# Kernel tuning notes

Hardware: AMD Instinct MI355X
Metric: run time of the kernel (lower is better)

## Reference

```python
import jax, jax.numpy as jnp
import numpy as np

# ---- t2t / fold geometry (FuseFormer defaults) ----
D_MODEL, HD = 512, 1960
K, S, P = 7, 3, 3            # kernel, stride, padding
H, W = 60, 108               # fold output_size
NH = (H + 2 * P - K) // S + 1  # 20
NW = (W + 2 * P - K) // S + 1  # 36
N_VECS = NH * NW             # 720
C = HD // (K * K)            # 40
HP, WP = H + 2 * P, W + 2 * P

# flat positions in the padded image for each (ki,kj,block_i,block_j)
_ki, _kj, _bi, _bj = np.meshgrid(np.arange(K), np.arange(K), np.arange(NH), np.arange(NW), indexing='ij')
POS = jnp.asarray(((_bi * S + _ki) * WP + (_bj * S + _kj)).reshape(-1))  # (K*K*N_VECS,)

# overlap-add count map (fold of all-ones normalizer), cropped to (H, W)
_cnt = np.zeros(HP * WP, dtype=np.float32)
np.add.at(_cnt, np.asarray(POS), 1.0)
NORM = jnp.asarray(_cnt.reshape(HP, WP)[P:P + H, P:P + W])  # (H, W), all > 0


def _fold_norm_unfold(h):
    # h: (B2, HD, N_VECS) -> fold -> divide by count -> unfold -> (B2, HD, N_VECS)
    B2 = h.shape[0]
    v = h.reshape(B2, C, K * K, N_VECS).reshape(B2, C, -1)
    img = jnp.zeros((B2, C, HP * WP), h.dtype).at[:, :, POS].add(v)
    img = img.reshape(B2, C, HP, WP)[:, :, P:P + H, P:P + W] / NORM  # crop + normalize
    imgp = jnp.pad(img, ((0, 0), (0, 0), (P, P), (P, P)))            # re-pad with zeros
    patches = imgp.reshape(B2, C, HP * WP)[:, :, POS]                # gather (unfold)
    return patches.reshape(B2, HD, N_VECS)


def setup_inputs() -> dict:
    key = jax.random.key(0)
    k1, k2, k3, k4, k5 = jax.random.split(key, 5)
    b, n = 4, 5 * N_VECS  # n = 3600
    return {
        'x': jax.random.normal(k1, (b, n, D_MODEL), jnp.float32),
        'W1': jax.random.normal(k2, (D_MODEL, HD), jnp.float32) * (1.0 / np.sqrt(D_MODEL)),
        'b1': jax.random.normal(k3, (HD,), jnp.float32) * 0.01,
        'W2': jax.random.normal(k4, (HD, D_MODEL), jnp.float32) * (1.0 / np.sqrt(HD)),
        'b2': jax.random.normal(k5, (D_MODEL,), jnp.float32) * 0.01,
    }


def reference(x, W1, b1, W2, b2):
    b, n, _ = x.shape
    h = jnp.einsum('bnd,dh->bnh', x, W1) + b1            # (b, n, HD)
    h = h.reshape(-1, N_VECS, HD).transpose(0, 2, 1)     # (B2, HD, N_VECS)
    h = _fold_norm_unfold(h)
    h = h.transpose(0, 2, 1).reshape(b, n, HD)
    out = jnp.einsum('bnh,hd->bnd', jax.nn.relu(h), W2) + b2  # dropout = identity (eval)
    return out
```

## Files before the change

kernel.cpp:

```cpp
#include <hip/hip_runtime.h>

#define D_MODEL 512
#define HD      1960
#define NPAD    2048
#define NVECS   720
#define MROWS   14400
#define MPAD    14464
#define HP      66
#define WP      114
#define IMGPIX  7524

typedef __bf16 bf16x8 __attribute__((ext_vector_type(8)));
typedef float  f32x4  __attribute__((ext_vector_type(4)));

__device__ __forceinline__ unsigned short f2bf(float f) {
    unsigned u = __builtin_bit_cast(unsigned, f);
    u += 0x7FFFu + ((u >> 16) & 1u);
    return (unsigned short)(u >> 16);
}
__device__ __forceinline__ float bf2f(unsigned short s) {
    unsigned u = ((unsigned)s) << 16;
    return __builtin_bit_cast(float, u);
}

__device__ __forceinline__ void gload_lds16(const unsigned short* g, unsigned short* l) {
    __builtin_amdgcn_global_load_lds(
        (const __attribute__((address_space(1))) unsigned int*)g,
        (__attribute__((address_space(3))) unsigned int*)l,
        16, 0, 0);
}

__global__ void cvt_x(const float* __restrict__ x, unsigned short* __restrict__ xb) {
    size_t i = ((size_t)blockIdx.x * 256 + threadIdx.x) * 4;
    const size_t valid = (size_t)MROWS * D_MODEL;
    if (i >= (size_t)MPAD * D_MODEL) return;
    ushort4 o;
    if (i < valid) {
        float4 v = *(const float4*)(x + i);
        o.x = f2bf(v.x); o.y = f2bf(v.y); o.z = f2bf(v.z); o.w = f2bf(v.w);
    } else {
        o.x = o.y = o.z = o.w = 0;
    }
    *(ushort4*)(xb + i) = o;
}

__global__ void transpose_cvt(const float* __restrict__ src, unsigned short* __restrict__ dst,
                              int srcR, int srcC, int dstR, int dstC) {
    __shared__ float tile[32][33];
    int c0 = blockIdx.x * 32;
    int r0 = blockIdx.y * 32;
    int tx = threadIdx.x, ty = threadIdx.y;
    #pragma unroll
    for (int i = 0; i < 32; i += 8) {
        int sr = c0 + ty + i, sc = r0 + tx;
        tile[ty + i][tx] = (sr < srcR && sc < srcC) ? src[(size_t)sr * srcC + sc] : 0.f;
    }
    __syncthreads();
    #pragma unroll
    for (int i = 0; i < 32; i += 8) {
        int dr = r0 + ty + i, dc = c0 + tx;
        if (dr < dstR && dc < dstC)
            dst[(size_t)dr * dstC + dc] = f2bf(tile[tx][ty + i]);
    }
}

template<int MODE>
__global__ void gemm_bt(const unsigned short* __restrict__ A,
                        const unsigned short* __restrict__ BT,
                        const float* __restrict__ bias,
                        void* __restrict__ Cout,
                        int K, int ldc, int validN, int validM) {
    __shared__ unsigned short smem[128 * 128];
    unsigned short* As = smem;
    unsigned short* Bs = smem + 128 * 64;
    const int t    = threadIdx.x;
    const int wid  = t >> 6, lane = t & 63;
    const int wr   = wid >> 1, wc = wid & 1;
    const int lr   = lane & 15, lh = lane >> 4;
    const int m0   = blockIdx.y * 128, n0 = blockIdx.x * 128;

    f32x4 acc[4][4] = {};

    const unsigned short* Aptr = A  + (size_t)(m0 + (t >> 3)) * K + (t & 7) * 8;
    const unsigned short* Bptr = BT + (size_t)(n0 + (t >> 3)) * K + (t & 7) * 8;
    unsigned short* Asl = As + t * 8;
    unsigned short* Bsl = Bs + t * 8;

    for (int kt = 0; kt < K; kt += 64) {
        #pragma unroll
        for (int i = 0; i < 4; ++i) {
            gload_lds16(Aptr + (size_t)(i * 32) * K + kt, Asl + i * 2048);
            gload_lds16(Bptr + (size_t)(i * 32) * K + kt, Bsl + i * 2048);
        }
        __syncthreads();
        #pragma unroll
        for (int ks = 0; ks < 2; ++ks) {
            bf16x8 a[4], b[4];
            #pragma unroll
            for (int f = 0; f < 4; ++f) {
                a[f] = *(const bf16x8*)&As[(wr * 64 + f * 16 + lr) * 64 + ks * 32 + lh * 8];
                b[f] = *(const bf16x8*)&Bs[(wc * 64 + f * 16 + lr) * 64 + ks * 32 + lh * 8];
            }
            #pragma unroll
            for (int fm = 0; fm < 4; ++fm)
                #pragma unroll
                for (int fn = 0; fn < 4; ++fn)
                    acc[fm][fn] = __builtin_amdgcn_mfma_f32_16x16x32_bf16(
                        a[fm], b[fn], acc[fm][fn], 0, 0, 0);
        }
        __syncthreads();
    }

    if (MODE == 0) {
        #pragma unroll
        for (int fm = 0; fm < 4; ++fm) {
            #pragma unroll
            for (int fn = 0; fn < 4; ++fn) {
                int lcol = wc * 64 + fn * 16 + lr;
                float bv = bias[n0 + lcol];
                #pragma unroll
                for (int j = 0; j < 4; ++j) {
                    int lrow = wr * 64 + fm * 16 + lh * 4 + j;
                    smem[lcol * 128 + (lrow ^ ((lcol & 15) << 3))] =
                        f2bf(acc[fm][fn][j] + bv);
                }
            }
        }
        __syncthreads();
        unsigned short* hT = (unsigned short*)Cout;
        int col = t >> 1, half = t & 1;
        int gcol = n0 + col;
        if (gcol < validN) {
            #pragma unroll
            for (int r = 0; r < 16; ++r) {
                int row = half * 64 + r * 4;
                ushort4 v4 = *(const ushort4*)&smem[col * 128 + (row ^ ((col & 15) << 3))];
                *(ushort4*)&hT[(size_t)gcol * MPAD + m0 + row] = v4;
            }
        }
    } else {
        #pragma unroll
        for (int fm = 0; fm < 4; ++fm) {
            #pragma unroll
            for (int fn = 0; fn < 4; ++fn) {
                int gcol = n0 + wc * 64 + fn * 16 + lr;
                float bv = bias[gcol];
                #pragma unroll
                for (int j = 0; j < 4; ++j) {
                    int grow = m0 + wr * 64 + fm * 16 + lh * 4 + j;
                    if (grow < validM)
                        ((float*)Cout)[(size_t)grow * ldc + gcol] = acc[fm][fn][j] + bv;
                }
            }
        }
    }
}

__global__ void fold_norm(const unsigned short* __restrict__ hT, unsigned short* __restrict__ img2) {
    int y  = blockIdx.x;
    int g  = blockIdx.y;
    int b2 = g / 10, cg = g % 10;
    int c0 = cg * 4;
    int x  = threadIdx.x;
    if (x >= WP) return;
    float val[4] = {0.f, 0.f, 0.f, 0.f};
    if (y >= 3 && y < 63 && x >= 3 && x < 111) {
        int kiA[3], biA[3], nki = 0;
        for (int ki = y % 3; ki < 7; ki += 3) {
            int bi = (y - ki) / 3;
            if (y - ki >= 0 && bi < 20) { kiA[nki] = ki; biA[nki] = bi; ++nki; }
        }
        int kjA[3], bjA[3], nkj = 0;
        for (int kj = x % 3; kj < 7; kj += 3) {
            int bj = (x - kj) / 3;
            if (x - kj >= 0 && bj < 36) { kjA[nkj] = kj; bjA[nkj] = bj; ++nkj; }
        }
        float s[4] = {0.f, 0.f, 0.f, 0.f};
        for (int i = 0; i < nki; ++i) {
            for (int j = 0; j < nkj; ++j) {
                int row = b2 * NVECS + biA[i] * 36 + bjA[j];
                int colb = kiA[i] * 7 + kjA[j];
                #pragma unroll
                for (int q = 0; q < 4; ++q)
                    s[q] += bf2f(hT[(size_t)((c0 + q) * 49 + colb) * MPAD + row]);
            }
        }
        float inv = 1.f / (float)(nki * nkj);
        #pragma unroll
        for (int q = 0; q < 4; ++q)
            val[q] = fmaxf(s[q] * inv, 0.f);
    }
    #pragma unroll
    for (int q = 0; q < 4; ++q)
        img2[(size_t)(b2 * 40 + c0 + q) * IMGPIX + y * WP + x] = f2bf(val[q]);
}

__global__ void unfold_k(const unsigned short* __restrict__ img2, unsigned short* __restrict__ h2b) {
    __shared__ unsigned short lds[20 * 798];
    __shared__ unsigned short lut[980];
    const int gb = blockIdx.x;
    const int cg = blockIdx.y;
    const int b2 = gb / 20, bi = gb % 20;
    const int t  = threadIdx.x;

    const unsigned short* src = img2 + (size_t)(b2 * 40 + cg * 20) * IMGPIX + (bi * 3) * WP;
    for (int p = t; p < 7980; p += 256) {
        int cc = p / 399, rem2 = p - cc * 399;
        *(ushort2*)&lds[cc * 798 + rem2 * 2] =
            *(const ushort2*)&src[(size_t)cc * IMGPIX + rem2 * 2];
    }
    for (int L = t; L < 980; L += 256) {
        int cc = L / 49, kk = L - cc * 49;
        lut[L] = (unsigned short)(cc * 798 + (kk / 7) * 114 + (kk % 7));
    }
    __syncthreads();

    const int cpr   = (cg == 0) ? 245 : 267;
    const int total = 36 * cpr;
    const int rowbase = b2 * NVECS + bi * 36;
    const int hdbase  = cg * 980;
    for (int i = t; i < total; i += 256) {
        int r = i / cpr, q = i - r * cpr;
        int hl = q * 4;
        ushort4 v;
        unsigned short* vv = (unsigned short*)&v;
        #pragma unroll
        for (int e = 0; e < 4; ++e) {
            int h = hl + e;
            vv[e] = (h < 980) ? lds[lut[h] + r * 3] : (unsigned short)0;
        }
        *(ushort4*)&h2b[(size_t)(rowbase + r) * NPAD + hdbase + hl] = v;
    }
}

extern "C" void kernel_launch(void* const* d_in, const int* in_sizes, int n_in,
                              void* d_out, int out_size, void* d_ws, size_t ws_size,
                              hipStream_t stream) {
    const float* x  = (const float*)d_in[0];
    const float* W1 = (const float*)d_in[1];
    const float* b1 = (const float*)d_in[2];
    const float* W2 = (const float*)d_in[3];
    const float* b2 = (const float*)d_in[4];
    float* out = (float*)d_out;

    unsigned short* xb   = (unsigned short*)d_ws;
    unsigned short* W1T  = xb   + (size_t)MPAD * D_MODEL;
    unsigned short* W2T  = W1T  + (size_t)NPAD * D_MODEL;
    unsigned short* hT   = W2T  + (size_t)D_MODEL * NPAD;
    unsigned short* h2b  = hT   + (size_t)NPAD * MPAD;
    unsigned short* img2 = h2b  + (size_t)MPAD * NPAD;

    cvt_x<<<(MPAD * D_MODEL / 4 + 255) / 256, 256, 0, stream>>>(x, xb);

    dim3 tb(32, 8);
    transpose_cvt<<<dim3(512 / 32, NPAD / 32), tb, 0, stream>>>(W1, W1T, D_MODEL, HD, NPAD, D_MODEL);
    transpose_cvt<<<dim3(NPAD / 32, 512 / 32), tb, 0, stream>>>(W2, W2T, HD, D_MODEL, D_MODEL, NPAD);

    gemm_bt<0><<<dim3(NPAD / 128, MPAD / 128), 256, 0, stream>>>(
        xb, W1T, b1, hT, D_MODEL, 0, HD, MPAD);

    fold_norm<<<dim3(HP, 200), 128, 0, stream>>>(hT, img2);
    unfold_k<<<dim3(400, 2), 256, 0, stream>>>(img2, h2b);

    gemm_bt<1><<<dim3(512 / 128, MPAD / 128), 256, 0, stream>>>(
        h2b, W2T, b2, out, NPAD, D_MODEL, D_MODEL, MROWS);
}
```

Before: 188.6 us.

## Use 256x256 double-buffered GEMM tiles and split-K for second GEMM

Both GEMMs move from 128x128 tiles with 256 threads to 256x256 tiles with 512 threads. The kernel double-buffers LDS with XOR-swizzled async global-to-LDS loads and uses explicit vmcnt waits and priority hints so loads overlap MFMA work. The second GEMM is split along K into two halves, with partial fp32 results written into the reused hT workspace and a new combine kernel that adds them together with the bias. MPAD grows so rows are a multiple of 256. In exchange, the 128 KB of LDS per block limits occupancy, and split-K adds extra partial-sum memory traffic plus one more launch.

```diff
diff --git a/kernel.cpp b/kernel.cpp
--- a/kernel.cpp
+++ b/kernel.cpp
@@ -5,7 +5,7 @@
 #define NPAD    2048
 #define NVECS   720
 #define MROWS   14400
-#define MPAD    14464
+#define MPAD    14592
 #define HP      66
 #define WP      114
 #define IMGPIX  7524
@@ -65,94 +65,140 @@
 }
 
 template<int MODE>
-__global__ void gemm_bt(const unsigned short* __restrict__ A,
-                        const unsigned short* __restrict__ BT,
-                        const float* __restrict__ bias,
-                        void* __restrict__ Cout,
-                        int K, int ldc, int validN, int validM) {
-    __shared__ unsigned short smem[128 * 128];
-    unsigned short* As = smem;
-    unsigned short* Bs = smem + 128 * 64;
+__global__ __launch_bounds__(512, 2) void gemm256(const unsigned short* __restrict__ A,
+                         const unsigned short* __restrict__ BT,
+                         const float* __restrict__ bias,
+                         void* __restrict__ Cout,
+                         int K, int NT, int validN) {
+    __shared__ unsigned short lds[65536];
     const int t    = threadIdx.x;
-    const int wid  = t >> 6, lane = t & 63;
-    const int wr   = wid >> 1, wc = wid & 1;
+    const int lane = t & 63;
+    const int wid  = t >> 6;
+    const int wr   = wid >> 2, wc = wid & 3;
     const int lr   = lane & 15, lh = lane >> 4;
-    const int m0   = blockIdx.y * 128, n0 = blockIdx.x * 128;
-
-    f32x4 acc[4][4] = {};
-
-    const unsigned short* Aptr = A  + (size_t)(m0 + (t >> 3)) * K + (t & 7) * 8;
-    const unsigned short* Bptr = BT + (size_t)(n0 + (t >> 3)) * K + (t & 7) * 8;
-    unsigned short* Asl = As + t * 8;
-    unsigned short* Bsl = Bs + t * 8;
-
-    for (int kt = 0; kt < K; kt += 64) {
-        #pragma unroll
-        for (int i = 0; i < 4; ++i) {
-            gload_lds16(Aptr + (size_t)(i * 32) * K + kt, Asl + i * 2048);
-            gload_lds16(Bptr + (size_t)(i * 32) * K + kt, Bsl + i * 2048);
-        }
+    const int m0   = blockIdx.y * 256, n0 = blockIdx.x * 256;
+    const int kz   = (MODE == 1) ? blockIdx.z : 0;
+    const unsigned short* Ab = A  + (size_t)kz * 1024;
+    const unsigned short* Bb = BT + (size_t)kz * 1024;
+
+    const int c0i = t,        r0i = c0i >> 3, q0 = (c0i & 7) ^ (r0i & 7);
+    const int c1i = t + 512,  r1i = c1i >> 3, q1 = (c1i & 7) ^ (r1i & 7);
+    const unsigned soffA00 = (unsigned)((m0 +       r0i) * K + q0 * 8);
+    const unsigned soffA01 = (unsigned)((m0 +       r1i) * K + q1 * 8);
+    const unsigned soffA10 = (unsigned)((m0 + 128 + r0i) * K + q0 * 8);
+    const unsigned soffA11 = (unsigned)((m0 + 128 + r1i) * K + q1 * 8);
+    const unsigned soffB00 = (unsigned)((n0 +       r0i) * K + q0 * 8);
+    const unsigned soffB01 = (unsigned)((n0 +       r1i) * K + q1 * 8);
+    const unsigned soffB10 = (unsigned)((n0 + 128 + r0i) * K + q0 * 8);
+    const unsigned soffB11 = (unsigned)((n0 + 128 + r1i) * K + q1 * 8);
+
+#define STAGE8(buf, kk) do { \
+        unsigned short* L = lds + (buf) * 32768; \
+        gload_lds16(Ab + soffA00 + (kk), L +         t * 8); \
+        gload_lds16(Ab + soffA01 + (kk), L +  4096 + t * 8); \
+        gload_lds16(Ab + soffA10 + (kk), L +  8192 + t * 8); \
+        gload_lds16(Ab + soffA11 + (kk), L + 12288 + t * 8); \
+        gload_lds16(Bb + soffB00 + (kk), L + 16384 +         t * 8); \
+        gload_lds16(Bb + soffB01 + (kk), L + 16384 +  4096 + t * 8); \
+        gload_lds16(Bb + soffB10 + (kk), L + 16384 +  8192 + t * 8); \
+        gload_lds16(Bb + soffB11 + (kk), L + 16384 + 12288 + t * 8); \
+    } while (0)
+
+    f32x4 acc[8][4] = {};
+
+    STAGE8(0, 0);
+    if (NT > 1) STAGE8(1, 64);
+
+    const int sl0 = lh ^ (lr & 7);
+    const int sl1 = sl0 ^ 4;
+
+    for (int kt = 0; kt < NT; ++kt) {
+        const int buf = kt & 1;
+        if (kt + 1 < NT) { asm volatile("s_waitcnt vmcnt(8)" ::: "memory"); }
+        else             { asm volatile("s_waitcnt vmcnt(0)" ::: "memory"); }
+        __builtin_amdgcn_s_barrier();
+        const unsigned short* La = lds + buf * 32768 + wr * 8192;
+        const unsigned short* Lb = lds + buf * 32768 + 16384 + (wc >> 1) * 8192 + (wc & 1) * 4096;
+        #pragma unroll
+        for (int ks = 0; ks < 2; ++ks) {
+            const int sl = ks ? sl1 : sl0;
+            bf16x8 a[8], b[4];
+            #pragma unroll
+            for (int f = 0; f < 8; ++f)
+                a[f] = *(const bf16x8*)(La + (f * 16 + lr) * 64 + sl * 8);
+            #pragma unroll
+            for (int g = 0; g < 4; ++g)
+                b[g] = *(const bf16x8*)(Lb + (g * 16 + lr) * 64 + sl * 8);
+            __builtin_amdgcn_s_setprio(1);
+            #pragma unroll
+            for (int f = 0; f < 8; ++f)
+                #pragma unroll
+                for (int g = 0; g < 4; ++g)
+                    acc[f][g] = __builtin_amdgcn_mfma_f32_16x16x32_bf16(a[f], b[g], acc[f][g], 0, 0, 0);
+            __builtin_amdgcn_s_setprio(0);
+        }
+        __builtin_amdgcn_s_barrier();
+        if (kt + 2 < NT) STAGE8(buf, (kt + 2) * 64);
+    }
+#undef STAGE8
+
+    if (MODE == 0) {
         __syncthreads();
         #pragma unroll
-        for (int ks = 0; ks < 2; ++ks) {
-            bf16x8 a[4], b[4];
-            #pragma unroll
-            for (int f = 0; f < 4; ++f) {
-                a[f] = *(const bf16x8*)&As[(wr * 64 + f * 16 + lr) * 64 + ks * 32 + lh * 8];
-                b[f] = *(const bf16x8*)&Bs[(wc * 64 + f * 16 + lr) * 64 + ks * 32 + lh * 8];
+        for (int f = 0; f < 8; ++f) {
+            #pragma unroll
+            for (int g = 0; g < 4; ++g) {
+                int col = wc * 64 + g * 16 + lr;
+                float bv = bias[n0 + col];
+                int gr = wr * 32 + f * 4 + lh;
+                ushort4 v4;
+                v4.x = f2bf(acc[f][g][0] + bv);
+                v4.y = f2bf(acc[f][g][1] + bv);
+                v4.z = f2bf(acc[f][g][2] + bv);
+                v4.w = f2bf(acc[f][g][3] + bv);
+                *(ushort4*)(lds + col * 256 + ((gr ^ (col & 63)) << 2)) = v4;
             }
-            #pragma unroll
-            for (int fm = 0; fm < 4; ++fm)
-                #pragma unroll
-                for (int fn = 0; fn < 4; ++fn)
-                    acc[fm][fn] = __builtin_amdgcn_mfma_f32_16x16x32_bf16(
-                        a[fm], b[fn], acc[fm][fn], 0, 0, 0);
         }
         __syncthreads();
-    }
-
-    if (MODE == 0) {
-        #pragma unroll
-        for (int fm = 0; fm < 4; ++fm) {
-            #pragma unroll
-            for (int fn = 0; fn < 4; ++fn) {
-                int lcol = wc * 64 + fn * 16 + lr;
-                float bv = bias[n0 + lcol];
+        unsigned short* hT = (unsigned short*)Cout;
+        int col = t & 255, half = t >> 8;
+        int gcol = n0 + col;
+        if (gcol < validN) {
+            #pragma unroll
+            for (int i = 0; i < 32; ++i) {
+                int gr = half * 32 + i;
+                ushort4 v4 = *(const ushort4*)(lds + col * 256 + ((gr ^ (col & 63)) << 2));
+                *(ushort4*)&hT[(size_t)gcol * MPAD + m0 + gr * 4] = v4;
+            }
+        }
+    } else {
+        float* P = (float*)Cout + (size_t)kz * ((size_t)MPAD * 512);
+        #pragma unroll
+        for (int f = 0; f < 8; ++f) {
+            #pragma unroll
+            for (int g = 0; g < 4; ++g) {
+                int gcol = n0 + wc * 64 + g * 16 + lr;
                 #pragma unroll
                 for (int j = 0; j < 4; ++j) {
-                    int lrow = wr * 64 + fm * 16 + lh * 4 + j;
-                    smem[lcol * 128 + (lrow ^ ((lcol & 15) << 3))] =
-                        f2bf(acc[fm][fn][j] + bv);
+                    int grow = m0 + wr * 128 + f * 16 + lh * 4 + j;
+                    P[(size_t)grow * 512 + gcol] = acc[f][g][j];
                 }
             }
         }
-        __syncthreads();
-        unsigned short* hT = (unsigned short*)Cout;
-        int col = t >> 1, half = t & 1;
-        int gcol = n0 + col;
-        if (gcol < validN) {
-            #pragma unroll
-            for (int r = 0; r < 16; ++r) {
-                int row = half * 64 + r * 4;
-                ushort4 v4 = *(const ushort4*)&smem[col * 128 + (row ^ ((col & 15) << 3))];
-                *(ushort4*)&hT[(size_t)gcol * MPAD + m0 + row] = v4;
-            }
-        }
-    } else {
-        #pragma unroll
-        for (int fm = 0; fm < 4; ++fm) {
-            #pragma unroll
-            for (int fn = 0; fn < 4; ++fn) {
-                int gcol = n0 + wc * 64 + fn * 16 + lr;
-                float bv = bias[gcol];
-                #pragma unroll
-                for (int j = 0; j < 4; ++j) {
-                    int grow = m0 + wr * 64 + fm * 16 + lh * 4 + j;
-                    if (grow < validM)
-                        ((float*)Cout)[(size_t)grow * ldc + gcol] = acc[fm][fn][j] + bv;
-                }
-            }
-        }
+    }
+}
+
+__global__ void combine_k(const float* __restrict__ P, const float* __restrict__ bias,
+                          float* __restrict__ out) {
+    const float* P1 = P + (size_t)MPAD * 512;
+    const size_t total = (size_t)MROWS * 512;
+    for (size_t i = ((size_t)blockIdx.x * 256 + threadIdx.x) * 4; i < total;
+         i += (size_t)gridDim.x * 256 * 4) {
+        float4 a = *(const float4*)(P + i);
+        float4 b = *(const float4*)(P1 + i);
+        float4 bv = *(const float4*)(bias + (i & 511));
+        float4 o = {a.x + b.x + bv.x, a.y + b.y + bv.y, a.z + b.z + bv.z, a.w + b.w + bv.w};
+        *(float4*)(out + i) = o;
     }
 }
 
@@ -256,12 +302,13 @@
     transpose_cvt<<<dim3(512 / 32, NPAD / 32), tb, 0, stream>>>(W1, W1T, D_MODEL, HD, NPAD, D_MODEL);
     transpose_cvt<<<dim3(NPAD / 32, 512 / 32), tb, 0, stream>>>(W2, W2T, HD, D_MODEL, D_MODEL, NPAD);
 
-    gemm_bt<0><<<dim3(NPAD / 128, MPAD / 128), 256, 0, stream>>>(
-        xb, W1T, b1, hT, D_MODEL, 0, HD, MPAD);
+    gemm256<0><<<dim3(NPAD / 256, MPAD / 256), 512, 0, stream>>>(
+        xb, W1T, b1, hT, D_MODEL, D_MODEL / 64, HD);
 
     fold_norm<<<dim3(HP, 200), 128, 0, stream>>>(hT, img2);
     unfold_k<<<dim3(400, 2), 256, 0, stream>>>(img2, h2b);
 
-    gemm_bt<1><<<dim3(512 / 128, MPAD / 128), 256, 0, stream>>>(
-        h2b, W2T, b2, out, NPAD, D_MODEL, D_MODEL, MROWS);
-}
+    gemm256<1><<<dim3(D_MODEL / 256, MPAD / 256, 2), 512, 0, stream>>>(
+        h2b, W2T, b2, hT, NPAD, 1024 / 64, D_MODEL);
+    combine_k<<<2048, 256, 0, stream>>>((const float*)hT, b2, out);
+}
```

New measurement: 189.7 us. About the same (+0.6%).

## Double-buffer GEMM LDS tiles with XOR swizzle and prefetch next K-tile

Applied to the files above, without the earlier changes.

The GEMM main loop now uses two LDS buffers. The next K-tile is issued via global-to-LDS loads before the current tile is computed, so memory latency overlaps with MFMA work. The LDS layout is XOR-swizzled on 16-byte chunks to reduce bank conflicts on fragment reads, and MFMA sections raise wave priority with s_setprio. LDS use doubles to 64KB per block, which may reduce occupancy, and the hand-written vmcnt waits assume exactly 8 outstanding loads per stage.

```diff
diff --git a/kernel.cpp b/kernel.cpp
--- a/kernel.cpp
+++ b/kernel.cpp
@@ -65,53 +65,82 @@
 }
 
 template<int MODE>
-__global__ void gemm_bt(const unsigned short* __restrict__ A,
+__global__ __launch_bounds__(256) void gemm_bt(const unsigned short* __restrict__ A,
                         const unsigned short* __restrict__ BT,
                         const float* __restrict__ bias,
                         void* __restrict__ Cout,
                         int K, int ldc, int validN, int validM) {
-    __shared__ unsigned short smem[128 * 128];
-    unsigned short* As = smem;
-    unsigned short* Bs = smem + 128 * 64;
+    __shared__ unsigned short lds[2][16384];
     const int t    = threadIdx.x;
     const int wid  = t >> 6, lane = t & 63;
     const int wr   = wid >> 1, wc = wid & 1;
     const int lr   = lane & 15, lh = lane >> 4;
     const int m0   = blockIdx.y * 128, n0 = blockIdx.x * 128;
 
+    int rr[4], qq[4];
+    #pragma unroll
+    for (int i = 0; i < 4; ++i) {
+        int c = t + i * 256;
+        rr[i] = c >> 3;
+        qq[i] = (c & 7) ^ (rr[i] & 7);
+    }
+
+#define STAGE(buf, kt) do { \
+        unsigned short* LA = &lds[buf][0]; \
+        unsigned short* LB = &lds[buf][8192]; \
+        _Pragma("unroll") \
+        for (int i = 0; i < 4; ++i) { \
+            gload_lds16(A  + (size_t)(m0 + rr[i]) * K + (kt) + qq[i] * 8, LA + (t + i * 256) * 8); \
+            gload_lds16(BT + (size_t)(n0 + rr[i]) * K + (kt) + qq[i] * 8, LB + (t + i * 256) * 8); \
+        } \
+    } while (0)
+
     f32x4 acc[4][4] = {};
-
-    const unsigned short* Aptr = A  + (size_t)(m0 + (t >> 3)) * K + (t & 7) * 8;
-    const unsigned short* Bptr = BT + (size_t)(n0 + (t >> 3)) * K + (t & 7) * 8;
-    unsigned short* Asl = As + t * 8;
-    unsigned short* Bsl = Bs + t * 8;
-
-    for (int kt = 0; kt < K; kt += 64) {
-        #pragma unroll
-        for (int i = 0; i < 4; ++i) {
-            gload_lds16(Aptr + (size_t)(i * 32) * K + kt, Asl + i * 2048);
-            gload_lds16(Bptr + (size_t)(i * 32) * K + kt, Bsl + i * 2048);
-        }
-        __syncthreads();
+    const int NT = K >> 6;
+
+    STAGE(0, 0);
+    for (int tt = 0; tt < NT; ++tt) {
+        if (tt + 1 < NT) {
+            STAGE((tt + 1) & 1, (tt + 1) * 64);
+            asm volatile("s_waitcnt vmcnt(8)" ::: "memory");
+        } else {
+            asm volatile("s_waitcnt vmcnt(0)" ::: "memory");
+        }
+        __builtin_amdgcn_s_barrier();
+        __builtin_amdgcn_sched_barrier(0);
+        const unsigned short* La = &lds[tt & 1][0];
+        const unsigned short* Lb = &lds[tt & 1][8192];
         #pragma unroll
         for (int ks = 0; ks < 2; ++ks) {
             bf16x8 a[4], b[4];
             #pragma unroll
             for (int f = 0; f < 4; ++f) {
-                a[f] = *(const bf16x8*)&As[(wr * 64 + f * 16 + lr) * 64 + ks * 32 + lh * 8];
-                b[f] = *(const bf16x8*)&Bs[(wc * 64 + f * 16 + lr) * 64 + ks * 32 + lh * 8];
-            }
+                int row = wr * 64 + f * 16 + lr;
+                int sl  = (ks * 4 + lh) ^ (lr & 7);
+                a[f] = *(const bf16x8*)(La + row * 64 + sl * 8);
+            }
+            #pragma unroll
+            for (int g = 0; g < 4; ++g) {
+                int row = wc * 64 + g * 16 + lr;
+                int sl  = (ks * 4 + lh) ^ (lr & 7);
+                b[g] = *(const bf16x8*)(Lb + row * 64 + sl * 8);
+            }
+            __builtin_amdgcn_s_setprio(1);
             #pragma unroll
             for (int fm = 0; fm < 4; ++fm)
                 #pragma unroll
                 for (int fn = 0; fn < 4; ++fn)
                     acc[fm][fn] = __builtin_amdgcn_mfma_f32_16x16x32_bf16(
                         a[fm], b[fn], acc[fm][fn], 0, 0, 0);
-        }
-        __syncthreads();
-    }
+            __builtin_amdgcn_s_setprio(0);
+        }
+        __builtin_amdgcn_s_barrier();
+        __builtin_amdgcn_sched_barrier(0);
+    }
+#undef STAGE
 
     if (MODE == 0) {
+        unsigned short* smem = &lds[0][0];
         #pragma unroll
         for (int fm = 0; fm < 4; ++fm) {
             #pragma unroll
```

Measured after the change: 177.9 us. 1.06x faster.
